# Optimization experiments

Hardware: AMD Instinct MI355X
Metric: run time of the kernel (lower is better)

The kernel has to match this reference:

```python
import jax, jax.numpy as jnp
import numpy as np

N_NODES = 20000
N_EDGES = 100000
N_SNAP = 2
N_DIM, E_DIM, OUT_DIM, HEADS = 64, 32, 64, 2


def edge_gat(x, ef, src, dst, Wn, We, al, ar, ae, b):
    # DGL EdgeGATConv: fc (no bias), edge-aware attention, edge softmax over
    # incoming edges, message = (ft_src + ft_edge) * alpha, final additive bias.
    H, D = al.shape
    ft = (x @ Wn).reshape(-1, H, D)                # [N,H,D]
    fe = (ef @ We).reshape(-1, H, D)               # [E,H,D]
    el = jnp.einsum('nhd,hd->nh', ft, al)          # [N,H]
    er = jnp.einsum('nhd,hd->nh', ft, ar)          # [N,H]
    ee = jnp.einsum('ehd,hd->eh', fe, ae)          # [E,H]
    logits = jax.nn.leaky_relu(el[src] + er[dst] + ee, 0.2)  # [E,H]
    m = jax.ops.segment_max(logits, dst, num_segments=N_NODES)
    p = jnp.exp(logits - m[dst])
    s = jax.ops.segment_sum(p, dst, num_segments=N_NODES)
    a = p / s[dst]                                 # edge softmax per dst node
    msg = (ft[src] + fe) * a[..., None]            # [E,H,D]
    return jax.ops.segment_sum(msg, dst, num_segments=N_NODES) + b  # [N,H,D]


def gnn_rnn(x, ef, src, dst, params):
    # GNN_RNN.forward per snapshot: stacked EdgeGAT layers, head-mean each.
    for (Wn, We, al, ar, ae, b) in params:
        x = edge_gat(x, ef, src, dst, Wn, We, al, ar, ae, b).mean(axis=1)
    return x


def _mk_layer(key, in_d, e_d, out_d, heads, scale=0.1):
    ks = jax.random.split(key, 6)
    return dict(
        Wn=jax.random.normal(ks[0], (in_d, heads * out_d), jnp.float32) * scale,
        We=jax.random.normal(ks[1], (e_d, heads * out_d), jnp.float32) * scale,
        al=jax.random.normal(ks[2], (heads, out_d), jnp.float32) * scale,
        ar=jax.random.normal(ks[3], (heads, out_d), jnp.float32) * scale,
        ae=jax.random.normal(ks[4], (heads, out_d), jnp.float32) * scale,
        b=jax.random.normal(ks[5], (heads, out_d), jnp.float32) * scale,
    )


def setup_inputs() -> dict:
    key = jax.random.key(0)
    ks = jax.random.split(key, 10)
    inp = {
        'x': jax.random.normal(ks[0], (N_SNAP, N_NODES, N_DIM), jnp.float32),
        'e': jax.random.normal(ks[1], (N_SNAP, N_EDGES, E_DIM), jnp.float32),
        'src': jax.random.randint(ks[2], (N_SNAP, N_EDGES), 0, N_NODES),
        'dst': jax.random.randint(ks[3], (N_SNAP, N_EDGES), 0, N_NODES),
    }
    enc0 = _mk_layer(ks[4], N_DIM, E_DIM, OUT_DIM, HEADS)
    enc1 = _mk_layer(ks[5], OUT_DIM, E_DIM, OUT_DIM, HEADS)
    dec0 = _mk_layer(ks[6], OUT_DIM, E_DIM, N_DIM, HEADS)
    dec1 = _mk_layer(ks[7], N_DIM, E_DIM, N_DIM, HEADS)
    for pref, lp in [('enc0', enc0), ('enc1', enc1), ('dec0', dec0), ('dec1', dec1)]:
        for k, v in lp.items():
            inp[f'{pref}_{k}'] = v
    inp['W_e2d'] = jax.random.normal(ks[8], (OUT_DIM, OUT_DIM), jnp.float32) * 0.1
    return inp


def reference(x, e, src, dst,
              enc0_Wn, enc0_We, enc0_al, enc0_ar, enc0_ae, enc0_b,
              enc1_Wn, enc1_We, enc1_al, enc1_ar, enc1_ae, enc1_b,
              W_e2d,
              dec0_Wn, dec0_We, dec0_al, dec0_ar, dec0_ae, dec0_b,
              dec1_Wn, dec1_We, dec1_al, dec1_ar, dec1_ae, dec1_b):
    enc_params = [(enc0_Wn, enc0_We, enc0_al, enc0_ar, enc0_ae, enc0_b),
                  (enc1_Wn, enc1_We, enc1_al, enc1_ar, enc1_ae, enc1_b)]
    dec_params = [(dec0_Wn, dec0_We, dec0_al, dec0_ar, dec0_ae, dec0_b),
                  (dec1_Wn, dec1_We, dec1_al, dec1_ar, dec1_ae, dec1_b)]

    def per_snapshot(xs, es, ss, ds):
        h = gnn_rnn(xs, es, ss, ds, enc_params)   # encoder, [N,out_dim]
        h = h @ W_e2d.T                           # encoder_to_decoder (no bias)
        return gnn_rnn(h, es, ss, ds, dec_params) # decoder, [N,n_dim]

    decoded = jax.vmap(per_snapshot)(x, e, src, dst)  # [S,N,n_dim]
    return decoded[-1]
```

## Files before the change

### kernel.cpp

```cpp
#include <hip/hip_runtime.h>
#include <math.h>

#define N_NODES 20000
#define N_EDGES 100000

__device__ __forceinline__ float rl_f(float v, int l) {
    return __uint_as_float(__builtin_amdgcn_readlane(__float_as_uint(v), l));
}
__device__ __forceinline__ int rl_i(int v, int l) {
    return __builtin_amdgcn_readlane(v, l);
}
__device__ __forceinline__ float lrelu(float x) { return x > 0.f ? x : 0.2f * x; }

__global__ __launch_bounds__(256) void count_kernel(const int* __restrict__ dst,
                                                    int* __restrict__ cnt,
                                                    int* __restrict__ pos) {
    int e = blockIdx.x * 256 + threadIdx.x;
    if (e < N_EDGES) pos[e] = atomicAdd(&cnt[dst[e]], 1);
}

__global__ __launch_bounds__(256) void scanA_kernel(const int* __restrict__ cnt,
                                                    int* __restrict__ bsum) {
    __shared__ int wsum[4];
    const int tid = threadIdx.x;
    int idx = blockIdx.x * 256 + tid;
    int v = (idx < N_NODES) ? cnt[idx] : 0;
    int s = v;
#pragma unroll
    for (int off = 32; off; off >>= 1) s += __shfl_xor(s, off);
    if ((tid & 63) == 0) wsum[tid >> 6] = s;
    __syncthreads();
    if (tid == 0) bsum[blockIdx.x] = wsum[0] + wsum[1] + wsum[2] + wsum[3];
}

__global__ __launch_bounds__(256) void scanC_kernel(const int* __restrict__ cnt,
                                                    const int* __restrict__ bsum,
                                                    int* __restrict__ row_ptr) {
    __shared__ int sdata[256];
    __shared__ int s_boff;
    const int tid = threadIdx.x;
    const int b = blockIdx.x;
    int idx = b * 256 + tid;
    int v = (idx < N_NODES) ? cnt[idx] : 0;
    sdata[tid] = v;
    if (tid < 64) {
        int a = (tid < b) ? bsum[tid] : 0;
        if (64 + tid < b) a += bsum[64 + tid];
#pragma unroll
        for (int off = 32; off; off >>= 1) a += __shfl_xor(a, off);
        if (tid == 0) s_boff = a;
    }
    __syncthreads();
    for (int off = 1; off < 256; off <<= 1) {
        int t_ = (tid >= off) ? sdata[tid - off] : 0;
        __syncthreads();
        sdata[tid] += t_;
        __syncthreads();
    }
    if (idx < N_NODES) row_ptr[idx] = s_boff + sdata[tid] - v;
    if (b == 0 && tid == 0) row_ptr[N_NODES] = N_EDGES;
}

__global__ __launch_bounds__(256) void params_kernel(
    const float* __restrict__ Wn0, const float* __restrict__ al0, const float* __restrict__ ar0,
    const float* __restrict__ Wn1, const float* __restrict__ al1, const float* __restrict__ ar1,
    const float* __restrict__ dWn, const float* __restrict__ al2, const float* __restrict__ ar2,
    const float* __restrict__ Wn3, const float* __restrict__ al3, const float* __restrict__ ar3,
    const float* __restrict__ W_e2d,
    const float* __restrict__ We0, const float* __restrict__ ae0,
    const float* __restrict__ We1, const float* __restrict__ ae1,
    const float* __restrict__ We2, const float* __restrict__ ae2,
    const float* __restrict__ We3, const float* __restrict__ ae3,
    const float* __restrict__ X0,
    float* __restrict__ P4, float* __restrict__ Wcomb, float* __restrict__ Q,
    float2* __restrict__ EL2, float2* __restrict__ ER2) {
    __shared__ float praw[256];
    const int b = blockIdx.x;
    const int t = threadIdx.x;

    if (b < 4) {
        const int L = b;
        if (L != 2) {
            const float* Wn = (L == 0) ? Wn0 : (L == 1) ? Wn1 : Wn3;
            const float* al = (L == 0) ? al0 : (L == 1) ? al1 : al3;
            const float* ar = (L == 0) ? ar0 : (L == 1) ? ar1 : ar3;
            const int k = t >> 2, o = t & 3;
            const float* a = (o & 2) ? ar : al;
            const int h = o & 1;
            float acc = 0.f;
#pragma unroll 8
            for (int d = 0; d < 64; d++) acc = fmaf(Wn[k * 128 + h * 64 + d], a[h * 64 + d], acc);
            P4[L * 256 + t] = acc;
        } else {
            {
                const int i = t >> 2, o = t & 3;
                const float* a = (o & 2) ? ar2 : al2;
                const int h = o & 1;
                float acc = 0.f;
#pragma unroll 8
                for (int d = 0; d < 64; d++) acc = fmaf(dWn[i * 128 + h * 64 + d], a[h * 64 + d], acc);
                praw[t] = acc;
            }
            __syncthreads();
            const int j = t >> 2, o = t & 3;
            float acc = 0.f;
#pragma unroll 8
            for (int i = 0; i < 64; i++) acc = fmaf(W_e2d[i * 64 + j], praw[i * 4 + o], acc);
            P4[2 * 256 + t] = acc;
        }
    } else if (b < 36) {
        int idx = (b - 4) * 256 + t;
        int j = idx >> 7, c = idx & 127;
        float acc = 0.f;
#pragma unroll 8
        for (int i = 0; i < 64; i++) acc = fmaf(W_e2d[i * 64 + j], dWn[i * 128 + c], acc);
        Wcomb[idx] = acc;
    } else if (b == 36) {
        const int k = t >> 3, o = t & 7, L = o >> 1, h = o & 1;
        const float* We = (L == 0) ? We0 : (L == 1) ? We1 : (L == 2) ? We2 : We3;
        const float* ae = (L == 0) ? ae0 : (L == 1) ? ae1 : (L == 2) ? ae2 : ae3;
        float acc = 0.f;
#pragma unroll 8
        for (int d = 0; d < 64; d++) acc = fmaf(We[k * 128 + h * 64 + d], ae[h * 64 + d], acc);
        Q[t] = acc;
    } else {
        {
            const int k = t >> 2, o = t & 3;
            const float* a = (o & 2) ? ar0 : al0;
            const int h = o & 1;
            float acc = 0.f;
#pragma unroll 8
            for (int d = 0; d < 64; d++) acc = fmaf(Wn0[k * 128 + h * 64 + d], a[h * 64 + d], acc);
            praw[t] = acc;
        }
        __syncthreads();
        const int lane = t & 63;
        const int wave = t >> 6;
        const float px = praw[lane * 4 + 0], py = praw[lane * 4 + 1];
        const float pz = praw[lane * 4 + 2], pw = praw[lane * 4 + 3];
        const int nb = gridDim.x - 37;
        for (int node = (b - 37) * 4 + wave; node < N_NODES; node += nb * 4) {
            float xv = X0[node * 64 + lane];
            float e0 = xv * px, e1 = xv * py, f0 = xv * pz, f1 = xv * pw;
#pragma unroll
            for (int off = 32; off; off >>= 1) {
                e0 += __shfl_xor(e0, off);
                e1 += __shfl_xor(e1, off);
                f0 += __shfl_xor(f0, off);
                f1 += __shfl_xor(f1, off);
            }
            if (lane == 0) {
                EL2[node] = make_float2(e0, e1);
                ER2[node] = make_float2(f0, f1);
            }
        }
    }
}

__global__ __launch_bounds__(256) void prep_kernel(const float* __restrict__ Efeat,
                                                   const int* __restrict__ src,
                                                   const int* __restrict__ dst,
                                                   const int* __restrict__ pos,
                                                   const int* __restrict__ row_ptr,
                                                   const float* __restrict__ Q,
                                                   float* __restrict__ E_csr,
                                                   int* __restrict__ src_csr,
                                                   float* __restrict__ EE_csr) {
    __shared__ float QS[256];
    __shared__ float ES[32][33];
    __shared__ int JS[32];
    const int tid = threadIdx.x;
    QS[tid] = Q[tid];
    const int e0 = blockIdx.x * 32;
    const int el_ = tid >> 3, quad = tid & 7;
    float4 v = ((const float4*)Efeat)[(size_t)(e0 + el_) * 8 + quad];
    ES[el_][quad * 4 + 0] = v.x;
    ES[el_][quad * 4 + 1] = v.y;
    ES[el_][quad * 4 + 2] = v.z;
    ES[el_][quad * 4 + 3] = v.w;
    if (tid < 32) {
        int e = e0 + tid;
        int j = row_ptr[dst[e]] + pos[e];
        JS[tid] = j;
        src_csr[j] = src[e];
    }
    __syncthreads();
    const int j = JS[el_];
    ((float4*)E_csr)[(size_t)j * 8 + quad] = v;
    const int o = quad;
    float acc = 0.f;
#pragma unroll
    for (int k = 0; k < 32; k++) acc = fmaf(ES[el_][k], QS[k * 8 + o], acc);
    EE_csr[(size_t)(o >> 1) * 2 * N_EDGES + (size_t)j * 2 + (o & 1)] = acc;
}

__global__ __launch_bounds__(256) void gather_kernel(const float* __restrict__ X,
                                                     const float2* __restrict__ EL2,
                                                     const float2* __restrict__ ER2,
                                                     const float* __restrict__ E_csr,
                                                     const int* __restrict__ src_csr,
                                                     const int* __restrict__ row_ptr,
                                                     const float2* __restrict__ EE_L,
                                                     float2* __restrict__ AX2,
                                                     float* __restrict__ AE) {
    const int tid = threadIdx.x;
    const int lane = tid & 63;
    const int node = blockIdx.x * 4 + (tid >> 6);
    if (node >= N_NODES) return;
    const int half = lane >> 5, hl = lane & 31;

    const int beg = row_ptr[node], end = row_ptr[node + 1];
    const int deg = end - beg;
    if (deg == 0) {
        AX2[node * 64 + lane] = make_float2(0.f, 0.f);
        AE[node * 64 + lane] = 0.f;
        return;
    }
    const float2 er = ER2[node];
    float l0 = 0.f, l1 = 0.f, aX0 = 0.f, aX1 = 0.f, aE = 0.f;

    if (deg <= 64) {
        int sn = 0;
        float w0 = 0.f, w1 = 0.f;
        if (lane < deg) {
            sn = src_csr[beg + lane];
            float2 ee = EE_L[beg + lane];
            float2 el = EL2[sn];
            w0 = __expf(lrelu(el.x + er.x + ee.x));
            w1 = __expf(lrelu(el.y + er.y + ee.y));
        }
        l0 = w0;
        l1 = w1;
#pragma unroll
        for (int off = 32; off; off >>= 1) {
            l0 += __shfl_xor(l0, off);
            l1 += __shfl_xor(l1, off);
        }
        const int dm1 = deg - 1;
        {
            float xs[8], es[8];
#pragma unroll
            for (int t = 0; t < 8; t++) {
                int ct = t < dm1 ? t : dm1;
                int st = rl_i(sn, ct);
                xs[t] = X[st * 64 + lane];
                es[t] = E_csr[(size_t)(beg + ct) * 32 + hl];
            }
#pragma unroll
            for (int t = 0; t < 8; t++) {
                float w0t = rl_f(w0, t);
                float w1t = rl_f(w1, t);
                aX0 = fmaf(w0t, xs[t], aX0);
                aX1 = fmaf(w1t, xs[t], aX1);
                aE = fmaf(half ? w1t : w0t, es[t], aE);
            }
        }
        int t = 8;
        for (; t + 4 <= deg; t += 4) {
            int s0 = rl_i(sn, t), s1 = rl_i(sn, t + 1);
            int s2 = rl_i(sn, t + 2), s3 = rl_i(sn, t + 3);
            float x0 = X[s0 * 64 + lane];
            float x1 = X[s1 * 64 + lane];
            float x2 = X[s2 * 64 + lane];
            float x3 = X[s3 * 64 + lane];
            const float* Eb = E_csr + (size_t)(beg + t) * 32 + hl;
            float e0 = Eb[0], e1 = Eb[32], e2 = Eb[64], e3 = Eb[96];
            float w00 = rl_f(w0, t), w01 = rl_f(w0, t + 1);
            float w02 = rl_f(w0, t + 2), w03 = rl_f(w0, t + 3);
            float w10 = rl_f(w1, t), w11 = rl_f(w1, t + 1);
            float w12 = rl_f(w1, t + 2), w13 = rl_f(w1, t + 3);
            aX0 = fmaf(w00, x0, aX0); aX1 = fmaf(w10, x0, aX1);
            aX0 = fmaf(w01, x1, aX0); aX1 = fmaf(w11, x1, aX1);
            aX0 = fmaf(w02, x2, aX0); aX1 = fmaf(w12, x2, aX1);
            aX0 = fmaf(w03, x3, aX0); aX1 = fmaf(w13, x3, aX1);
            aE = fmaf(half ? w10 : w00, e0, aE);
            aE = fmaf(half ? w11 : w01, e1, aE);
            aE = fmaf(half ? w12 : w02, e2, aE);
            aE = fmaf(half ? w13 : w03, e3, aE);
        }
        for (; t < deg; t++) {
            int st = rl_i(sn, t);
            float w0t = rl_f(w0, t), w1t = rl_f(w1, t);
            float xv = X[st * 64 + lane];
            float ev = E_csr[(size_t)(beg + t) * 32 + hl];
            aX0 = fmaf(w0t, xv, aX0);
            aX1 = fmaf(w1t, xv, aX1);
            aE = fmaf(half ? w1t : w0t, ev, aE);
        }
    } else {
        for (int c = beg; c < end; c += 64) {
            int j = c + lane;
            int sn_ = 0;
            float w0c = 0.f, w1c = 0.f;
            if (j < end) {
                sn_ = src_csr[j];
                float2 ee = EE_L[j];
                float2 el = EL2[sn_];
                w0c = __expf(lrelu(el.x + er.x + ee.x));
                w1c = __expf(lrelu(el.y + er.y + ee.y));
            }
            float s0 = w0c, s1 = w1c;
#pragma unroll
            for (int off = 32; off; off >>= 1) {
                s0 += __shfl_xor(s0, off);
                s1 += __shfl_xor(s1, off);
            }
            l0 += s0;
            l1 += s1;
            int nch = (end - c) < 64 ? (end - c) : 64;
            int t = 0;
            for (; t + 4 <= nch; t += 4) {
                int q0 = rl_i(sn_, t), q1 = rl_i(sn_, t + 1);
                int q2 = rl_i(sn_, t + 2), q3 = rl_i(sn_, t + 3);
                float x0 = X[q0 * 64 + lane];
                float x1 = X[q1 * 64 + lane];
                float x2 = X[q2 * 64 + lane];
                float x3 = X[q3 * 64 + lane];
                const float* Eb = E_csr + (size_t)(c + t) * 32 + hl;
                float e0 = Eb[0], e1 = Eb[32], e2 = Eb[64], e3 = Eb[96];
                float w00 = rl_f(w0c, t), w01 = rl_f(w0c, t + 1);
                float w02 = rl_f(w0c, t + 2), w03 = rl_f(w0c, t + 3);
                float w10 = rl_f(w1c, t), w11 = rl_f(w1c, t + 1);
                float w12 = rl_f(w1c, t + 2), w13 = rl_f(w1c, t + 3);
                aX0 = fmaf(w00, x0, aX0); aX1 = fmaf(w10, x0, aX1);
                aX0 = fmaf(w01, x1, aX0); aX1 = fmaf(w11, x1, aX1);
                aX0 = fmaf(w02, x2, aX0); aX1 = fmaf(w12, x2, aX1);
                aX0 = fmaf(w03, x3, aX0); aX1 = fmaf(w13, x3, aX1);
                aE = fmaf(half ? w10 : w00, e0, aE);
                aE = fmaf(half ? w11 : w01, e1, aE);
                aE = fmaf(half ? w12 : w02, e2, aE);
                aE = fmaf(half ? w13 : w03, e3, aE);
            }
            for (; t < nch; t++) {
                int st = rl_i(sn_, t);
                float w0t = rl_f(w0c, t), w1t = rl_f(w1c, t);
                float xv = X[st * 64 + lane];
                float ev = E_csr[(size_t)(c + t) * 32 + hl];
                aX0 = fmaf(w0t, xv, aX0);
                aX1 = fmaf(w1t, xv, aX1);
                aE = fmaf(half ? w1t : w0t, ev, aE);
            }
        }
    }
    const float inv0 = l0 > 0.f ? 1.f / l0 : 0.f;
    const float inv1 = l1 > 0.f ? 1.f / l1 : 0.f;
    AX2[node * 64 + lane] = make_float2(aX0 * inv0, aX1 * inv1);
    AE[node * 64 + lane] = aE * (half ? inv1 : inv0);
}

__global__ __launch_bounds__(256) void epilogue_kernel(const float2* __restrict__ AX2,
                                                       const float* __restrict__ AE,
                                                       const float* __restrict__ Wn,
                                                       const float* __restrict__ We,
                                                       const float* __restrict__ bias,
                                                       const float* __restrict__ P4next,
                                                       const int has_next,
                                                       float* __restrict__ OUT,
                                                       float2* __restrict__ EL2,
                                                       float2* __restrict__ ER2) {
    __shared__ float4 WnS4[32 * 64];
    __shared__ float4 WeS4[16 * 64];
    const int tid = threadIdx.x;
    for (int idx = tid; idx < 32 * 64; idx += 256) {
        int k2 = idx >> 6, l = idx & 63;
        WnS4[idx] = make_float4(Wn[(2 * k2) * 128 + l], Wn[(2 * k2) * 128 + 64 + l],
                                Wn[(2 * k2 + 1) * 128 + l], Wn[(2 * k2 + 1) * 128 + 64 + l]);
    }
    for (int idx = tid; idx < 16 * 64; idx += 256) {
        int k2 = idx >> 6, l = idx & 63;
        WeS4[idx] = make_float4(We[(2 * k2) * 128 + l], We[(2 * k2) * 128 + 64 + l],
                                We[(2 * k2 + 1) * 128 + l], We[(2 * k2 + 1) * 128 + 64 + l]);
    }
    __syncthreads();
    const int lane = tid & 63;
    const int wave = tid >> 6;
    const float b0 = bias[lane], b1 = bias[64 + lane];
    const float4 p = has_next ? ((const float4*)P4next)[lane] : make_float4(0.f, 0.f, 0.f, 0.f);

    for (int base = blockIdx.x * 8 + wave * 2; base < N_NODES; base += gridDim.x * 8) {
        const int n0 = base, n1 = base + 1;
        float2 axa = AX2[n0 * 64 + lane];
        float2 axb = AX2[n1 * 64 + lane];
        float aea = AE[n0 * 64 + lane];
        float aeb = AE[n1 * 64 + lane];
        float r0a = 0.f, r1a = 0.f, r0b = 0.f, r1b = 0.f;
#pragma unroll
        for (int k2 = 0; k2 < 32; k2++) {
            float4 w4 = WnS4[k2 * 64 + lane];
            float a00 = rl_f(axa.x, 2 * k2), a01 = rl_f(axa.x, 2 * k2 + 1);
            float a10 = rl_f(axa.y, 2 * k2), a11 = rl_f(axa.y, 2 * k2 + 1);
            float c00 = rl_f(axb.x, 2 * k2), c01 = rl_f(axb.x, 2 * k2 + 1);
            float c10 = rl_f(axb.y, 2 * k2), c11 = rl_f(axb.y, 2 * k2 + 1);
            r0a = fmaf(a00, w4.x, r0a); r1a = fmaf(a10, w4.y, r1a);
            r0a = fmaf(a01, w4.z, r0a); r1a = fmaf(a11, w4.w, r1a);
            r0b = fmaf(c00, w4.x, r0b); r1b = fmaf(c10, w4.y, r1b);
            r0b = fmaf(c01, w4.z, r0b); r1b = fmaf(c11, w4.w, r1b);
        }
#pragma unroll
        for (int k2 = 0; k2 < 16; k2++) {
            float4 w4 = WeS4[k2 * 64 + lane];
            float a00 = rl_f(aea, 2 * k2), a01 = rl_f(aea, 2 * k2 + 1);
            float a10 = rl_f(aea, 32 + 2 * k2), a11 = rl_f(aea, 32 + 2 * k2 + 1);
            float c00 = rl_f(aeb, 2 * k2), c01 = rl_f(aeb, 2 * k2 + 1);
            float c10 = rl_f(aeb, 32 + 2 * k2), c11 = rl_f(aeb, 32 + 2 * k2 + 1);
            r0a = fmaf(a00, w4.x, r0a); r1a = fmaf(a10, w4.y, r1a);
            r0a = fmaf(a01, w4.z, r0a); r1a = fmaf(a11, w4.w, r1a);
            r0b = fmaf(c00, w4.x, r0b); r1b = fmaf(c10, w4.y, r1b);
            r0b = fmaf(c01, w4.z, r0b); r1b = fmaf(c11, w4.w, r1b);
        }
        float outa = 0.5f * (r0a + b0 + r1a + b1);
        float outb = 0.5f * (r0b + b0 + r1b + b1);
        OUT[n0 * 64 + lane] = outa;
        OUT[n1 * 64 + lane] = outb;
        if (has_next) {
            float e0a = outa * p.x, e1a = outa * p.y, f0a = outa * p.z, f1a = outa * p.w;
            float e0b = outb * p.x, e1b = outb * p.y, f0b = outb * p.z, f1b = outb * p.w;
#pragma unroll
            for (int off = 32; off; off >>= 1) {
                e0a += __shfl_xor(e0a, off); e1a += __shfl_xor(e1a, off);
                f0a += __shfl_xor(f0a, off); f1a += __shfl_xor(f1a, off);
                e0b += __shfl_xor(e0b, off); e1b += __shfl_xor(e1b, off);
                f0b += __shfl_xor(f0b, off); f1b += __shfl_xor(f1b, off);
            }
            if (lane == 0) {
                EL2[n0] = make_float2(e0a, e1a);
                ER2[n0] = make_float2(f0a, f1a);
                EL2[n1] = make_float2(e0b, e1b);
                ER2[n1] = make_float2(f0b, f1b);
            }
        }
    }
}

extern "C" void kernel_launch(void* const* d_in, const int* in_sizes, int n_in,
                              void* d_out, int out_size, void* d_ws, size_t ws_size,
                              hipStream_t stream) {
    const float* x = (const float*)d_in[0];
    const float* e = (const float*)d_in[1];
    const int* src = (const int*)d_in[2];
    const int* dst = (const int*)d_in[3];

    const float* x1 = x + (size_t)1 * N_NODES * 64;
    const float* e1 = e + (size_t)1 * N_EDGES * 32;
    const int* src1 = src + N_EDGES;
    const int* dst1 = dst + N_EDGES;

    int we2d_idx, dec0_b, dec1_b;
    if (in_sizes[16] == 64 * 64 && in_sizes[17] == 64 * 128) {
        we2d_idx = 16; dec0_b = 17; dec1_b = 23;
    } else {
        dec0_b = 16; dec1_b = 22; we2d_idx = 28;
    }
    auto P = [&](int i) { return (const float*)d_in[i]; };

    char* ws = (char*)d_ws;
    int* cnt      = (int*)(ws + 0);
    int* row_ptr  = (int*)(ws + 80000);
    int* pos      = (int*)(ws + 160064);
    int* bsum     = (int*)(ws + 560064);
    float* q      = (float*)(ws + 560576);
    int* src_csr  = (int*)(ws + 561600);
    float* e_csr  = (float*)(ws + 961600);
    float* ee_csr = (float*)(ws + 13761600);
    float* p4_all = (float*)(ws + 16961600);
    float* el     = (float*)(ws + 16965696);
    float* er     = (float*)(ws + 17125696);
    float* ax     = (float*)(ws + 17285696);
    float* ae     = (float*)(ws + 27525696);
    float* h      = (float*)(ws + 32645696);
    float* wcomb  = (float*)(ws + 37765696);

    hipMemsetAsync(cnt, 0, N_NODES * sizeof(int), stream);
    const int EB = (N_EDGES + 255) / 256;
    const int SB = (N_NODES + 255) / 256;
    count_kernel<<<EB, 256, 0, stream>>>(dst1, cnt, pos);
    scanA_kernel<<<SB, 256, 0, stream>>>(cnt, bsum);
    scanC_kernel<<<SB, 256, 0, stream>>>(cnt, bsum, row_ptr);

    params_kernel<<<512, 256, 0, stream>>>(
        P(4), P(6), P(7),
        P(10), P(12), P(13),
        P(dec0_b + 0), P(dec0_b + 2), P(dec0_b + 3),
        P(dec1_b + 0), P(dec1_b + 2), P(dec1_b + 3),
        P(we2d_idx),
        P(5), P(8), P(11), P(14),
        P(dec0_b + 1), P(dec0_b + 4), P(dec1_b + 1), P(dec1_b + 4),
        x1,
        p4_all, wcomb, q, (float2*)el, (float2*)er);

    prep_kernel<<<N_EDGES / 32, 256, 0, stream>>>(e1, src1, dst1, pos, row_ptr, q,
                                                  e_csr, src_csr, ee_csr);

    const int NB_G = (N_NODES + 3) / 4;
    const int NB_E = 768;

    auto run_layer = [&](const float* Xin, const float* Wn, const float* We_,
                         const float* b_, int L, float* Out) {
        gather_kernel<<<NB_G, 256, 0, stream>>>(
            Xin, (const float2*)el, (const float2*)er, e_csr, src_csr, row_ptr,
            (const float2*)(ee_csr) + (size_t)L * N_EDGES, (float2*)ax, ae);
        epilogue_kernel<<<NB_E, 256, 0, stream>>>(
            (const float2*)ax, ae, Wn, We_, b_, p4_all + (L + 1) * 256, (L < 3) ? 1 : 0,
            Out, (float2*)el, (float2*)er);
    };

    run_layer(x1, P(4), P(5), P(9), 0, h);
    run_layer(h, P(10), P(11), P(15), 1, h);
    run_layer(h, wcomb, P(dec0_b + 1), P(dec0_b + 5), 2, h);
    run_layer(h, P(dec1_b + 0), P(dec1_b + 1), P(dec1_b + 5), 3, (float*)d_out);
}
```

Measured before the change: 310.8 us.

## Fuse per-layer gather and epilogue into one kernel with prepacked weights

Merges the gather (softmax-weighted aggregation) and epilogue (projection, bias, next-layer attention terms) kernels into a single persistent layer kernel. Aggregated features stay in registers instead of round-tripping through global AX/AE buffers. Weights are packed once into a float4 layout in the setup kernel so each block copies them straight into shared memory. Edge counting is folded into the setup kernel, and EL/ER buffers are double-buffered so reads and writes do not race. The cost is 48KB of shared memory per block, which may limit occupancy for the latency-bound gather loop.

Measured after the change: 317.8 us. 2.3% more time.

```diff
diff --git a/kernel.cpp b/kernel.cpp
--- a/kernel.cpp
+++ b/kernel.cpp
@@ -11,13 +11,6 @@
     return __builtin_amdgcn_readlane(v, l);
 }
 __device__ __forceinline__ float lrelu(float x) { return x > 0.f ? x : 0.2f * x; }
-
-__global__ __launch_bounds__(256) void count_kernel(const int* __restrict__ dst,
-                                                    int* __restrict__ cnt,
-                                                    int* __restrict__ pos) {
-    int e = blockIdx.x * 256 + threadIdx.x;
-    if (e < N_EDGES) pos[e] = atomicAdd(&cnt[dst[e]], 1);
-}
 
 __global__ __launch_bounds__(256) void scanA_kernel(const int* __restrict__ cnt,
                                                     int* __restrict__ bsum) {
@@ -61,7 +54,8 @@
     if (b == 0 && tid == 0) row_ptr[N_NODES] = N_EDGES;
 }
 
-__global__ __launch_bounds__(256) void params_kernel(
+__global__ __launch_bounds__(256) void setup_kernel(
+    const int* __restrict__ dst, int* __restrict__ cnt, int* __restrict__ pos,
     const float* __restrict__ Wn0, const float* __restrict__ al0, const float* __restrict__ ar0,
     const float* __restrict__ Wn1, const float* __restrict__ al1, const float* __restrict__ ar1,
     const float* __restrict__ dWn, const float* __restrict__ al2, const float* __restrict__ ar2,
@@ -72,11 +66,18 @@
     const float* __restrict__ We2, const float* __restrict__ ae2,
     const float* __restrict__ We3, const float* __restrict__ ae3,
     const float* __restrict__ X0,
-    float* __restrict__ P4, float* __restrict__ Wcomb, float* __restrict__ Q,
+    float* __restrict__ P4, float* __restrict__ Q, float4* __restrict__ Wpack,
     float2* __restrict__ EL2, float2* __restrict__ ER2) {
     __shared__ float praw[256];
-    const int b = blockIdx.x;
     const int t = threadIdx.x;
+    const int bb = blockIdx.x;
+
+    if (bb < 391) {
+        int e = bb * 256 + t;
+        if (e < N_EDGES) pos[e] = atomicAdd(&cnt[dst[e]], 1);
+        return;
+    }
+    const int b = bb - 391;
 
     if (b < 4) {
         const int L = b;
@@ -108,14 +109,7 @@
             for (int i = 0; i < 64; i++) acc = fmaf(W_e2d[i * 64 + j], praw[i * 4 + o], acc);
             P4[2 * 256 + t] = acc;
         }
-    } else if (b < 36) {
-        int idx = (b - 4) * 256 + t;
-        int j = idx >> 7, c = idx & 127;
-        float acc = 0.f;
-#pragma unroll 8
-        for (int i = 0; i < 64; i++) acc = fmaf(W_e2d[i * 64 + j], dWn[i * 128 + c], acc);
-        Wcomb[idx] = acc;
-    } else if (b == 36) {
+    } else if (b == 4) {
         const int k = t >> 3, o = t & 7, L = o >> 1, h = o & 1;
         const float* We = (L == 0) ? We0 : (L == 1) ? We1 : (L == 2) ? We2 : We3;
         const float* ae = (L == 0) ? ae0 : (L == 1) ? ae1 : (L == 2) ? ae2 : ae3;
@@ -123,6 +117,36 @@
 #pragma unroll 8
         for (int d = 0; d < 64; d++) acc = fmaf(We[k * 128 + h * 64 + d], ae[h * 64 + d], acc);
         Q[t] = acc;
+    } else if (b < 53) {
+        const int idx = (b - 5) * 256 + t;
+        const int L = idx / 3072;
+        const int sub = idx - L * 3072;
+        if (sub < 2048) {
+            const int k2 = sub >> 6, l = sub & 63;
+            if (L != 2) {
+                const float* Wn = (L == 0) ? Wn0 : (L == 1) ? Wn1 : Wn3;
+                Wpack[idx] = make_float4(Wn[(2 * k2) * 128 + l], Wn[(2 * k2) * 128 + 64 + l],
+                                         Wn[(2 * k2 + 1) * 128 + l], Wn[(2 * k2 + 1) * 128 + 64 + l]);
+            } else {
+                float a0 = 0.f, a1 = 0.f, a2 = 0.f, a3 = 0.f;
+#pragma unroll 4
+                for (int i = 0; i < 64; i++) {
+                    float wa = W_e2d[i * 64 + 2 * k2], wb = W_e2d[i * 64 + 2 * k2 + 1];
+                    float da = dWn[i * 128 + l], db = dWn[i * 128 + 64 + l];
+                    a0 = fmaf(wa, da, a0);
+                    a1 = fmaf(wa, db, a1);
+                    a2 = fmaf(wb, da, a2);
+                    a3 = fmaf(wb, db, a3);
+                }
+                Wpack[idx] = make_float4(a0, a1, a2, a3);
+            }
+        } else {
+            const int s2 = sub - 2048;
+            const int k2 = s2 >> 6, l = s2 & 63;
+            const float* We = (L == 0) ? We0 : (L == 1) ? We1 : (L == 2) ? We2 : We3;
+            Wpack[idx] = make_float4(We[(2 * k2) * 128 + l], We[(2 * k2) * 128 + 64 + l],
+                                     We[(2 * k2 + 1) * 128 + l], We[(2 * k2 + 1) * 128 + 64 + l]);
+        }
     } else {
         {
             const int k = t >> 2, o = t & 3;
@@ -138,8 +162,8 @@
         const int wave = t >> 6;
         const float px = praw[lane * 4 + 0], py = praw[lane * 4 + 1];
         const float pz = praw[lane * 4 + 2], pw = praw[lane * 4 + 3];
-        const int nb = gridDim.x - 37;
-        for (int node = (b - 37) * 4 + wave; node < N_NODES; node += nb * 4) {
+        const int nb = (int)gridDim.x - 444;
+        for (int node = (b - 53) * 4 + wave; node < N_NODES; node += nb * 4) {
             float xv = X0[node * 64 + lane];
             float e0 = xv * px, e1 = xv * py, f0 = xv * pz, f1 = xv * pw;
 #pragma unroll
@@ -194,239 +218,195 @@
     EE_csr[(size_t)(o >> 1) * 2 * N_EDGES + (size_t)j * 2 + (o & 1)] = acc;
 }
 
-__global__ __launch_bounds__(256) void gather_kernel(const float* __restrict__ X,
-                                                     const float2* __restrict__ EL2,
-                                                     const float2* __restrict__ ER2,
-                                                     const float* __restrict__ E_csr,
-                                                     const int* __restrict__ src_csr,
-                                                     const int* __restrict__ row_ptr,
-                                                     const float2* __restrict__ EE_L,
-                                                     float2* __restrict__ AX2,
-                                                     float* __restrict__ AE) {
+__global__ __launch_bounds__(256) void layer_kernel(
+    const float* __restrict__ X,
+    const float2* __restrict__ ELi, const float2* __restrict__ ERi,
+    const float* __restrict__ E_csr, const int* __restrict__ src_csr,
+    const int* __restrict__ row_ptr, const float2* __restrict__ EE_L,
+    const float4* __restrict__ Wp, const float* __restrict__ bias,
+    const float* __restrict__ P4next, const int has_next,
+    float* __restrict__ OUT,
+    float2* __restrict__ ELo, float2* __restrict__ ERo) {
+    __shared__ float4 WS[3072];
     const int tid = threadIdx.x;
-    const int lane = tid & 63;
-    const int node = blockIdx.x * 4 + (tid >> 6);
-    if (node >= N_NODES) return;
-    const int half = lane >> 5, hl = lane & 31;
-
-    const int beg = row_ptr[node], end = row_ptr[node + 1];
-    const int deg = end - beg;
-    if (deg == 0) {
-        AX2[node * 64 + lane] = make_float2(0.f, 0.f);
-        AE[node * 64 + lane] = 0.f;
-        return;
-    }
-    const float2 er = ER2[node];
-    float l0 = 0.f, l1 = 0.f, aX0 = 0.f, aX1 = 0.f, aE = 0.f;
-
-    if (deg <= 64) {
-        int sn = 0;
-        float w0 = 0.f, w1 = 0.f;
-        if (lane < deg) {
-            sn = src_csr[beg + lane];
-            float2 ee = EE_L[beg + lane];
-            float2 el = EL2[sn];
-            w0 = __expf(lrelu(el.x + er.x + ee.x));
-            w1 = __expf(lrelu(el.y + er.y + ee.y));
-        }
-        l0 = w0;
-        l1 = w1;
-#pragma unroll
-        for (int off = 32; off; off >>= 1) {
-            l0 += __shfl_xor(l0, off);
-            l1 += __shfl_xor(l1, off);
-        }
-        const int dm1 = deg - 1;
-        {
-            float xs[8], es[8];
-#pragma unroll
-            for (int t = 0; t < 8; t++) {
-                int ct = t < dm1 ? t : dm1;
-                int st = rl_i(sn, ct);
-                xs[t] = X[st * 64 + lane];
-                es[t] = E_csr[(size_t)(beg + ct) * 32 + hl];
-            }
-#pragma unroll
-            for (int t = 0; t < 8; t++) {
-                float w0t = rl_f(w0, t);
-                float w1t = rl_f(w1, t);
-                aX0 = fmaf(w0t, xs[t], aX0);
-                aX1 = fmaf(w1t, xs[t], aX1);
-                aE = fmaf(half ? w1t : w0t, es[t], aE);
-            }
-        }
-        int t = 8;
-        for (; t + 4 <= deg; t += 4) {
-            int s0 = rl_i(sn, t), s1 = rl_i(sn, t + 1);
-            int s2 = rl_i(sn, t + 2), s3 = rl_i(sn, t + 3);
-            float x0 = X[s0 * 64 + lane];
-            float x1 = X[s1 * 64 + lane];
-            float x2 = X[s2 * 64 + lane];
-            float x3 = X[s3 * 64 + lane];
-            const float* Eb = E_csr + (size_t)(beg + t) * 32 + hl;
-            float e0 = Eb[0], e1 = Eb[32], e2 = Eb[64], e3 = Eb[96];
-            float w00 = rl_f(w0, t), w01 = rl_f(w0, t + 1);
-            float w02 = rl_f(w0, t + 2), w03 = rl_f(w0, t + 3);
-            float w10 = rl_f(w1, t), w11 = rl_f(w1, t + 1);
-            float w12 = rl_f(w1, t + 2), w13 = rl_f(w1, t + 3);
-            aX0 = fmaf(w00, x0, aX0); aX1 = fmaf(w10, x0, aX1);
-            aX0 = fmaf(w01, x1, aX0); aX1 = fmaf(w11, x1, aX1);
-            aX0 = fmaf(w02, x2, aX0); aX1 = fmaf(w12, x2, aX1);
-            aX0 = fmaf(w03, x3, aX0); aX1 = fmaf(w13, x3, aX1);
-            aE = fmaf(half ? w10 : w00, e0, aE);
-            aE = fmaf(half ? w11 : w01, e1, aE);
-            aE = fmaf(half ? w12 : w02, e2, aE);
-            aE = fmaf(half ? w13 : w03, e3, aE);
-        }
-        for (; t < deg; t++) {
-            int st = rl_i(sn, t);
-            float w0t = rl_f(w0, t), w1t = rl_f(w1, t);
-            float xv = X[st * 64 + lane];
-            float ev = E_csr[(size_t)(beg + t) * 32 + hl];
-            aX0 = fmaf(w0t, xv, aX0);
-            aX1 = fmaf(w1t, xv, aX1);
-            aE = fmaf(half ? w1t : w0t, ev, aE);
-        }
-    } else {
-        for (int c = beg; c < end; c += 64) {
-            int j = c + lane;
-            int sn_ = 0;
-            float w0c = 0.f, w1c = 0.f;
-            if (j < end) {
-                sn_ = src_csr[j];
-                float2 ee = EE_L[j];
-                float2 el = EL2[sn_];
-                w0c = __expf(lrelu(el.x + er.x + ee.x));
-                w1c = __expf(lrelu(el.y + er.y + ee.y));
-            }
-            float s0 = w0c, s1 = w1c;
-#pragma unroll
-            for (int off = 32; off; off >>= 1) {
-                s0 += __shfl_xor(s0, off);
-                s1 += __shfl_xor(s1, off);
-            }
-            l0 += s0;
-            l1 += s1;
-            int nch = (end - c) < 64 ? (end - c) : 64;
-            int t = 0;
-            for (; t + 4 <= nch; t += 4) {
-                int q0 = rl_i(sn_, t), q1 = rl_i(sn_, t + 1);
-                int q2 = rl_i(sn_, t + 2), q3 = rl_i(sn_, t + 3);
-                float x0 = X[q0 * 64 + lane];
-                float x1 = X[q1 * 64 + lane];
-                float x2 = X[q2 * 64 + lane];
-                float x3 = X[q3 * 64 + lane];
-                const float* Eb = E_csr + (size_t)(c + t) * 32 + hl;
-                float e0 = Eb[0], e1 = Eb[32], e2 = Eb[64], e3 = Eb[96];
-                float w00 = rl_f(w0c, t), w01 = rl_f(w0c, t + 1);
-                float w02 = rl_f(w0c, t + 2), w03 = rl_f(w0c, t + 3);
-                float w10 = rl_f(w1c, t), w11 = rl_f(w1c, t + 1);
-                float w12 = rl_f(w1c, t + 2), w13 = rl_f(w1c, t + 3);
-                aX0 = fmaf(w00, x0, aX0); aX1 = fmaf(w10, x0, aX1);
-                aX0 = fmaf(w01, x1, aX0); aX1 = fmaf(w11, x1, aX1);
-                aX0 = fmaf(w02, x2, aX0); aX1 = fmaf(w12, x2, aX1);
-                aX0 = fmaf(w03, x3, aX0); aX1 = fmaf(w13, x3, aX1);
-                aE = fmaf(half ? w10 : w00, e0, aE);
-                aE = fmaf(half ? w11 : w01, e1, aE);
-                aE = fmaf(half ? w12 : w02, e2, aE);
-                aE = fmaf(half ? w13 : w03, e3, aE);
-            }
-            for (; t < nch; t++) {
-                int st = rl_i(sn_, t);
-                float w0t = rl_f(w0c, t), w1t = rl_f(w1c, t);
-                float xv = X[st * 64 + lane];
-                float ev = E_csr[(size_t)(c + t) * 32 + hl];
-                aX0 = fmaf(w0t, xv, aX0);
-                aX1 = fmaf(w1t, xv, aX1);
-                aE = fmaf(half ? w1t : w0t, ev, aE);
-            }
-        }
-    }
-    const float inv0 = l0 > 0.f ? 1.f / l0 : 0.f;
-    const float inv1 = l1 > 0.f ? 1.f / l1 : 0.f;
-    AX2[node * 64 + lane] = make_float2(aX0 * inv0, aX1 * inv1);
-    AE[node * 64 + lane] = aE * (half ? inv1 : inv0);
-}
-
-__global__ __launch_bounds__(256) void epilogue_kernel(const float2* __restrict__ AX2,
-                                                       const float* __restrict__ AE,
-                                                       const float* __restrict__ Wn,
-                                                       const float* __restrict__ We,
-                                                       const float* __restrict__ bias,
-                                                       const float* __restrict__ P4next,
-                                                       const int has_next,
-                                                       float* __restrict__ OUT,
-                                                       float2* __restrict__ EL2,
-                                                       float2* __restrict__ ER2) {
-    __shared__ float4 WnS4[32 * 64];
-    __shared__ float4 WeS4[16 * 64];
-    const int tid = threadIdx.x;
-    for (int idx = tid; idx < 32 * 64; idx += 256) {
-        int k2 = idx >> 6, l = idx & 63;
-        WnS4[idx] = make_float4(Wn[(2 * k2) * 128 + l], Wn[(2 * k2) * 128 + 64 + l],
-                                Wn[(2 * k2 + 1) * 128 + l], Wn[(2 * k2 + 1) * 128 + 64 + l]);
-    }
-    for (int idx = tid; idx < 16 * 64; idx += 256) {
-        int k2 = idx >> 6, l = idx & 63;
-        WeS4[idx] = make_float4(We[(2 * k2) * 128 + l], We[(2 * k2) * 128 + 64 + l],
-                                We[(2 * k2 + 1) * 128 + l], We[(2 * k2 + 1) * 128 + 64 + l]);
-    }
-    __syncthreads();
+#pragma unroll
+    for (int i = 0; i < 12; i++) WS[i * 256 + tid] = Wp[i * 256 + tid];
+
     const int lane = tid & 63;
     const int wave = tid >> 6;
-    const float b0 = bias[lane], b1 = bias[64 + lane];
+    const int half = lane >> 5, hl = lane & 31;
+    const float bb0 = bias[lane], bb1 = bias[64 + lane];
     const float4 p = has_next ? ((const float4*)P4next)[lane] : make_float4(0.f, 0.f, 0.f, 0.f);
-
-    for (int base = blockIdx.x * 8 + wave * 2; base < N_NODES; base += gridDim.x * 8) {
-        const int n0 = base, n1 = base + 1;
-        float2 axa = AX2[n0 * 64 + lane];
-        float2 axb = AX2[n1 * 64 + lane];
-        float aea = AE[n0 * 64 + lane];
-        float aeb = AE[n1 * 64 + lane];
-        float r0a = 0.f, r1a = 0.f, r0b = 0.f, r1b = 0.f;
+    __syncthreads();
+
+    const int stride = gridDim.x * 4;
+    for (int node = blockIdx.x * 4 + wave; node < N_NODES; node += stride) {
+        const int beg = row_ptr[node], end = row_ptr[node + 1];
+        const int deg = end - beg;
+        float ax0 = 0.f, ax1 = 0.f, aeh = 0.f;
+        if (deg > 0) {
+            const float2 er = ERi[node];
+            float l0 = 0.f, l1 = 0.f, aX0 = 0.f, aX1 = 0.f, aE = 0.f;
+            if (deg <= 64) {
+                int sn = 0;
+                float w0 = 0.f, w1 = 0.f;
+                if (lane < deg) {
+                    sn = src_csr[beg + lane];
+                    float2 ee = EE_L[beg + lane];
+                    float2 el = ELi[sn];
+                    w0 = __expf(lrelu(el.x + er.x + ee.x));
+                    w1 = __expf(lrelu(el.y + er.y + ee.y));
+                }
+                l0 = w0;
+                l1 = w1;
+#pragma unroll
+                for (int off = 32; off; off >>= 1) {
+                    l0 += __shfl_xor(l0, off);
+                    l1 += __shfl_xor(l1, off);
+                }
+                const int dm1 = deg - 1;
+                {
+                    float xs[8], es[8];
+#pragma unroll
+                    for (int t = 0; t < 8; t++) {
+                        int ct = t < dm1 ? t : dm1;
+                        int st = rl_i(sn, ct);
+                        xs[t] = X[st * 64 + lane];
+                        es[t] = E_csr[(size_t)(beg + ct) * 32 + hl];
+                    }
+#pragma unroll
+                    for (int t = 0; t < 8; t++) {
+                        float w0t = rl_f(w0, t);
+                        float w1t = rl_f(w1, t);
+                        aX0 = fmaf(w0t, xs[t], aX0);
+                        aX1 = fmaf(w1t, xs[t], aX1);
+                        aE = fmaf(half ? w1t : w0t, es[t], aE);
+                    }
+                }
+                int t = 8;
+                for (; t + 4 <= deg; t += 4) {
+                    int s0 = rl_i(sn, t), s1 = rl_i(sn, t + 1);
+                    int s2 = rl_i(sn, t + 2), s3 = rl_i(sn, t + 3);
+                    float x0 = X[s0 * 64 + lane];
+                    float x1 = X[s1 * 64 + lane];
+                    float x2 = X[s2 * 64 + lane];
+                    float x3 = X[s3 * 64 + lane];
+                    const float* Eb = E_csr + (size_t)(beg + t) * 32 + hl;
+                    float e0 = Eb[0], e1 = Eb[32], e2 = Eb[64], e3 = Eb[96];
+                    float w00 = rl_f(w0, t), w01 = rl_f(w0, t + 1);
+                    float w02 = rl_f(w0, t + 2), w03 = rl_f(w0, t + 3);
+                    float w10 = rl_f(w1, t), w11 = rl_f(w1, t + 1);
+                    float w12 = rl_f(w1, t + 2), w13 = rl_f(w1, t + 3);
+                    aX0 = fmaf(w00, x0, aX0); aX1 = fmaf(w10, x0, aX1);
+                    aX0 = fmaf(w01, x1, aX0); aX1 = fmaf(w11, x1, aX1);
+                    aX0 = fmaf(w02, x2, aX0); aX1 = fmaf(w12, x2, aX1);
+                    aX0 = fmaf(w03, x3, aX0); aX1 = fmaf(w13, x3, aX1);
+                    aE = fmaf(half ? w10 : w00, e0, aE);
+                    aE = fmaf(half ? w11 : w01, e1, aE);
+                    aE = fmaf(half ? w12 : w02, e2, aE);
+                    aE = fmaf(half ? w13 : w03, e3, aE);
+                }
+                for (; t < deg; t++) {
+                    int st = rl_i(sn, t);
+                    float w0t = rl_f(w0, t), w1t = rl_f(w1, t);
+                    float xv = X[st * 64 + lane];
+                    float ev = E_csr[(size_t)(beg + t) * 32 + hl];
+                    aX0 = fmaf(w0t, xv, aX0);
+                    aX1 = fmaf(w1t, xv, aX1);
+                    aE = fmaf(half ? w1t : w0t, ev, aE);
+                }
+            } else {
+                for (int c = beg; c < end; c += 64) {
+                    int jj = c + lane;
+                    int sn_ = 0;
+                    float w0c = 0.f, w1c = 0.f;
+                    if (jj < end) {
+                        sn_ = src_csr[jj];
+                        float2 ee = EE_L[jj];
+                        float2 el = ELi[sn_];
+                        w0c = __expf(lrelu(el.x + er.x + ee.x));
+                        w1c = __expf(lrelu(el.y + er.y + ee.y));
+                    }
+                    float s0_ = w0c, s1_ = w1c;
+#pragma unroll
+                    for (int off = 32; off; off >>= 1) {
+                        s0_ += __shfl_xor(s0_, off);
+                        s1_ += __shfl_xor(s1_, off);
+                    }
+                    l0 += s0_;
+                    l1 += s1_;
+                    int nch = (end - c) < 64 ? (end - c) : 64;
+                    int t = 0;
+                    for (; t + 4 <= nch; t += 4) {
+                        int q0 = rl_i(sn_, t), q1 = rl_i(sn_, t + 1);
+                        int q2 = rl_i(sn_, t + 2), q3 = rl_i(sn_, t + 3);
+                        float x0 = X[q0 * 64 + lane];
+                        float x1 = X[q1 * 64 + lane];
+                        float x2 = X[q2 * 64 + lane];
+                        float x3 = X[q3 * 64 + lane];
+                        const float* Eb = E_csr + (size_t)(c + t) * 32 + hl;
+                        float e0 = Eb[0], e1 = Eb[32], e2 = Eb[64], e3 = Eb[96];
+                        float w00 = rl_f(w0c, t), w01 = rl_f(w0c, t + 1);
+                        float w02 = rl_f(w0c, t + 2), w03 = rl_f(w0c, t + 3);
+                        float w10 = rl_f(w1c, t), w11 = rl_f(w1c, t + 1);
+                        float w12 = rl_f(w1c, t + 2), w13 = rl_f(w1c, t + 3);
+                        aX0 = fmaf(w00, x0, aX0); aX1 = fmaf(w10, x0, aX1);
+                        aX0 = fmaf(w01, x1, aX0); aX1 = fmaf(w11, x1, aX1);
+                        aX0 = fmaf(w02, x2, aX0); aX1 = fmaf(w12, x2, aX1);
+                        aX0 = fmaf(w03, x3, aX0); aX1 = fmaf(w13, x3, aX1);
+                        aE = fmaf(half ? w10 : w00, e0, aE);
+                        aE = fmaf(half ? w11 : w01, e1, aE);
+                        aE = fmaf(half ? w12 : w02, e2, aE);
+                        aE = fmaf(half ? w13 : w03, e3, aE);
+                    }
+                    for (; t < nch; t++) {
+                        int st = rl_i(sn_, t);
+                        float w0t = rl_f(w0c, t), w1t = rl_f(w1c, t);
+                        float xv = X[st * 64 + lane];
+                        float ev = E_csr[(size_t)(c + t) * 32 + hl];
+                        aX0 = fmaf(w0t, xv, aX0);
+                        aX1 = fmaf(w1t, xv, aX1);
+                        aE = fmaf(half ? w1t : w0t, ev, aE);
+                    }
+                }
+            }
+            const float inv0 = l0 > 0.f ? 1.f / l0 : 0.f;
+            const float inv1 = l1 > 0.f ? 1.f / l1 : 0.f;
+            ax0 = aX0 * inv0;
+            ax1 = aX1 * inv1;
+            aeh = aE * (half ? inv1 : inv0);
+        }
+        float r0 = 0.f, r1 = 0.f;
 #pragma unroll
         for (int k2 = 0; k2 < 32; k2++) {
-            float4 w4 = WnS4[k2 * 64 + lane];
-            float a00 = rl_f(axa.x, 2 * k2), a01 = rl_f(axa.x, 2 * k2 + 1);
-            float a10 = rl_f(axa.y, 2 * k2), a11 = rl_f(axa.y, 2 * k2 + 1);
-            float c00 = rl_f(axb.x, 2 * k2), c01 = rl_f(axb.x, 2 * k2 + 1);
-            float c10 = rl_f(axb.y, 2 * k2), c11 = rl_f(axb.y, 2 * k2 + 1);
-            r0a = fmaf(a00, w4.x, r0a); r1a = fmaf(a10, w4.y, r1a);
-            r0a = fmaf(a01, w4.z, r0a); r1a = fmaf(a11, w4.w, r1a);
-            r0b = fmaf(c00, w4.x, r0b); r1b = fmaf(c10, w4.y, r1b);
-            r0b = fmaf(c01, w4.z, r0b); r1b = fmaf(c11, w4.w, r1b);
+            float4 w4 = WS[k2 * 64 + lane];
+            r0 = fmaf(rl_f(ax0, 2 * k2), w4.x, r0);
+            r1 = fmaf(rl_f(ax1, 2 * k2), w4.y, r1);
+            r0 = fmaf(rl_f(ax0, 2 * k2 + 1), w4.z, r0);
+            r1 = fmaf(rl_f(ax1, 2 * k2 + 1), w4.w, r1);
         }
 #pragma unroll
         for (int k2 = 0; k2 < 16; k2++) {
-            float4 w4 = WeS4[k2 * 64 + lane];
-            float a00 = rl_f(aea, 2 * k2), a01 = rl_f(aea, 2 * k2 + 1);
-            float a10 = rl_f(aea, 32 + 2 * k2), a11 = rl_f(aea, 32 + 2 * k2 + 1);
-            float c00 = rl_f(aeb, 2 * k2), c01 = rl_f(aeb, 2 * k2 + 1);
-            float c10 = rl_f(aeb, 32 + 2 * k2), c11 = rl_f(aeb, 32 + 2 * k2 + 1);
-            r0a = fmaf(a00, w4.x, r0a); r1a = fmaf(a10, w4.y, r1a);
-            r0a = fmaf(a01, w4.z, r0a); r1a = fmaf(a11, w4.w, r1a);
-            r0b = fmaf(c00, w4.x, r0b); r1b = fmaf(c10, w4.y, r1b);
-            r0b = fmaf(c01, w4.z, r0b); r1b = fmaf(c11, w4.w, r1b);
-        }
-        float outa = 0.5f * (r0a + b0 + r1a + b1);
-        float outb = 0.5f * (r0b + b0 + r1b + b1);
-        OUT[n0 * 64 + lane] = outa;
-        OUT[n1 * 64 + lane] = outb;
+            float4 w4 = WS[2048 + k2 * 64 + lane];
+            r0 = fmaf(rl_f(aeh, 2 * k2), w4.x, r0);
+            r1 = fmaf(rl_f(aeh, 32 + 2 * k2), w4.y, r1);
+            r0 = fmaf(rl_f(aeh, 2 * k2 + 1), w4.z, r0);
+            r1 = fmaf(rl_f(aeh, 32 + 2 * k2 + 1), w4.w, r1);
+        }
+        const float outv = 0.5f * (r0 + bb0 + r1 + bb1);
+        OUT[node * 64 + lane] = outv;
         if (has_next) {
-            float e0a = outa * p.x, e1a = outa * p.y, f0a = outa * p.z, f1a = outa * p.w;
-            float e0b = outb * p.x, e1b = outb * p.y, f0b = outb * p.z, f1b = outb * p.w;
+            float e0 = outv * p.x, e1 = outv * p.y, f0 = outv * p.z, f1 = outv * p.w;
 #pragma unroll
             for (int off = 32; off; off >>= 1) {
-                e0a += __shfl_xor(e0a, off); e1a += __shfl_xor(e1a, off);
-                f0a += __shfl_xor(f0a, off); f1a += __shfl_xor(f1a, off);
-                e0b += __shfl_xor(e0b, off); e1b += __shfl_xor(e1b, off);
-                f0b += __shfl_xor(f0b, off); f1b += __shfl_xor(f1b, off);
+                e0 += __shfl_xor(e0, off);
+                e1 += __shfl_xor(e1, off);
+                f0 += __shfl_xor(f0, off);
+                f1 += __shfl_xor(f1, off);
             }
             if (lane == 0) {
-                EL2[n0] = make_float2(e0a, e1a);
-                ER2[n0] = make_float2(f0a, f1a);
-                EL2[n1] = make_float2(e0b, e1b);
-                ER2[n1] = make_float2(f0b, f1b);
+                ELo[node] = make_float2(e0, e1);
+                ERo[node] = make_float2(f0, f1);
             }
         }
     }
@@ -463,21 +443,18 @@
     float* e_csr  = (float*)(ws + 961600);
     float* ee_csr = (float*)(ws + 13761600);
     float* p4_all = (float*)(ws + 16961600);
-    float* el     = (float*)(ws + 16965696);
-    float* er     = (float*)(ws + 17125696);
-    float* ax     = (float*)(ws + 17285696);
-    float* ae     = (float*)(ws + 27525696);
-    float* h      = (float*)(ws + 32645696);
-    float* wcomb  = (float*)(ws + 37765696);
+    float* elA    = (float*)(ws + 16965696);
+    float* erA    = (float*)(ws + 17125696);
+    float* elB    = (float*)(ws + 17285696);
+    float* erB    = (float*)(ws + 17445696);
+    float* h0     = (float*)(ws + 17605696);
+    float* h1     = (float*)(ws + 22725696);
+    float4* wpack = (float4*)(ws + 27845696);
 
     hipMemsetAsync(cnt, 0, N_NODES * sizeof(int), stream);
-    const int EB = (N_EDGES + 255) / 256;
-    const int SB = (N_NODES + 255) / 256;
-    count_kernel<<<EB, 256, 0, stream>>>(dst1, cnt, pos);
-    scanA_kernel<<<SB, 256, 0, stream>>>(cnt, bsum);
-    scanC_kernel<<<SB, 256, 0, stream>>>(cnt, bsum, row_ptr);
-
-    params_kernel<<<512, 256, 0, stream>>>(
+
+    setup_kernel<<<903, 256, 0, stream>>>(
+        dst1, cnt, pos,
         P(4), P(6), P(7),
         P(10), P(12), P(13),
         P(dec0_b + 0), P(dec0_b + 2), P(dec0_b + 3),
@@ -486,26 +463,30 @@
         P(5), P(8), P(11), P(14),
         P(dec0_b + 1), P(dec0_b + 4), P(dec1_b + 1), P(dec1_b + 4),
         x1,
-        p4_all, wcomb, q, (float2*)el, (float2*)er);
+        p4_all, q, wpack, (float2*)elA, (float2*)erA);
+
+    const int SB = (N_NODES + 255) / 256;
+    scanA_kernel<<<SB, 256, 0, stream>>>(cnt, bsum);
+    scanC_kernel<<<SB, 256, 0, stream>>>(cnt, bsum, row_ptr);
 
     prep_kernel<<<N_EDGES / 32, 256, 0, stream>>>(e1, src1, dst1, pos, row_ptr, q,
                                                   e_csr, src_csr, ee_csr);
 
-    const int NB_G = (N_NODES + 3) / 4;
-    const int NB_E = 768;
-
-    auto run_layer = [&](const float* Xin, const float* Wn, const float* We_,
-                         const float* b_, int L, float* Out) {
-        gather_kernel<<<NB_G, 256, 0, stream>>>(
-            Xin, (const float2*)el, (const float2*)er, e_csr, src_csr, row_ptr,
-            (const float2*)(ee_csr) + (size_t)L * N_EDGES, (float2*)ax, ae);
-        epilogue_kernel<<<NB_E, 256, 0, stream>>>(
-            (const float2*)ax, ae, Wn, We_, b_, p4_all + (L + 1) * 256, (L < 3) ? 1 : 0,
-            Out, (float2*)el, (float2*)er);
+    const int NB_L = 1024;
+    auto run = [&](const float* Xin, int L, const float* bias_,
+                   const float* elI, const float* erI,
+                   float* Out, float* elO, float* erO, int hn) {
+        layer_kernel<<<NB_L, 256, 0, stream>>>(
+            Xin, (const float2*)elI, (const float2*)erI,
+            e_csr, src_csr, row_ptr,
+            (const float2*)ee_csr + (size_t)L * N_EDGES,
+            wpack + (size_t)L * 3072, bias_,
+            p4_all + (L + 1) * 256, hn,
+            Out, (float2*)elO, (float2*)erO);
     };
 
-    run_layer(x1, P(4), P(5), P(9), 0, h);
-    run_layer(h, P(10), P(11), P(15), 1, h);
-    run_layer(h, wcomb, P(dec0_b + 1), P(dec0_b + 5), 2, h);
-    run_layer(h, P(dec1_b + 0), P(dec1_b + 1), P(dec1_b + 5), 3, (float*)d_out);
-}
+    run(x1, 0, P(9),           elA, erA, h0, elB, erB, 1);
+    run(h0, 1, P(15),          elB, erB, h1, elA, erA, 1);
+    run(h1, 2, P(dec0_b + 5),  elA, erA, h0, elB, erB, 1);
+    run(h0, 3, P(dec1_b + 5),  elB, erB, (float*)d_out, elA, erA, 0);
+}
```
